# Kernel optimization log

Measured on AMD Instinct MI355X. Metric: run time of the kernel, lower is better.

Reference implementation:

```python
import jax, jax.numpy as jnp
import numpy as np

# ---- dims (match init_kwargs) ----
IMG = 128; PATCH = 16; GRID = IMG // PATCH; L = GRID * GRID  # 64 patches
D = 256            # embed_dim
EXP = 2; DIN = D * EXP          # d_inner = 512
DH = 64; H = DIN // DH          # 8 heads
G = 1; N = 64                   # n_groups, d_state
DCONV = 4
DEPTH = 2
NCLS = 1000
BATCH = 16
DINPROJ = 2 * DIN + 2 * G * N + H   # z | xBC | dt
CDIM = DIN + 2 * G * N              # conv channels
EPS = 1e-6

def _snake_indices():
    g = np.arange(L).reshape(GRID, GRID)
    g[1::2] = g[1::2, ::-1]
    return jnp.asarray(g.reshape(-1))

SNAKE = _snake_indices()

def rmsnorm(x, w):
    return x * jax.lax.rsqrt(jnp.mean(x * x, axis=-1, keepdims=True) + EPS) * w

def causal_depthwise_conv(x, w, b):
    # x: (B,L,C), w: (C,K) depthwise causal conv, then SiLU
    xp = jnp.pad(x, ((0, 0), (DCONV - 1, 0), (0, 0)))
    y = sum(xp[:, k:k + x.shape[1], :] * w[:, k] for k in range(DCONV))
    return jax.nn.silu(y + b)

def mamba_block(x, Win, cw, cb, dtb, Alog, Dp, gn, Wout):
    # Mamba-2/3 style selective scan block. x: (B,L,D)
    Bsz, Lx, _ = x.shape
    zxbcdt = x @ Win                                   # (B,L,DINPROJ)
    z   = zxbcdt[..., :DIN]
    xBC = zxbcdt[..., DIN:DIN + CDIM]
    dt  = jax.nn.softplus(zxbcdt[..., DIN + CDIM:] + dtb)   # (B,L,H)
    xBC = causal_depthwise_conv(xBC, cw, cb)
    xs = xBC[..., :DIN].reshape(Bsz, Lx, H, DH)
    Bm = xBC[..., DIN:DIN + G * N].reshape(Bsz, Lx, G, N)
    Cm = xBC[..., DIN + G * N:].reshape(Bsz, Lx, G, N)
    Bh = jnp.repeat(Bm, H // G, axis=2)                # (B,L,H,N)
    Ch = jnp.repeat(Cm, H // G, axis=2)
    decay = jnp.exp(dt * (-jnp.exp(Alog)))             # (B,L,H) in (0,1)
    dBx = jnp.einsum('blh,blhp,blhn->blhpn', dt, xs, Bh)
    def step(h, inp):
        d, u = inp
        h = d[..., None, None] * h + u
        return h, h
    _, hs = jax.lax.scan(step, jnp.zeros((Bsz, H, DH, N), x.dtype),
                         (jnp.moveaxis(decay, 1, 0), jnp.moveaxis(dBx, 1, 0)))
    hs = jnp.moveaxis(hs, 0, 1)                        # (B,L,H,DH,N)
    y = jnp.einsum('blhpn,blhn->blhp', hs, Ch) + Dp[None, None, :, None] * xs
    y = y.reshape(Bsz, Lx, DIN)
    y = rmsnorm(y * jax.nn.silu(z), gn)                # gated RMSNorm
    return y @ Wout                                    # (B,L,D)

def setup_inputs() -> dict:
    key = jax.random.key(0)
    ks = jax.random.split(key, 24)
    s_in = 1.0 / np.sqrt(D); s_out = 1.0 / np.sqrt(DIN)
    def blk(k):
        kk = jax.random.split(k, 8)
        return dict(
            Win=jax.random.normal(kk[0], (DEPTH, D, DINPROJ)) * s_in,
            cw=jax.random.normal(kk[1], (DEPTH, CDIM, DCONV)) * 0.3,
            cb=jnp.zeros((DEPTH, CDIM)),
            dtb=jax.random.normal(kk[2], (DEPTH, H)) * 0.1,
            Alog=jnp.log(jax.random.uniform(kk[3], (DEPTH, H), minval=1.0, maxval=16.0)),
            Dp=jnp.ones((DEPTH, H)),
            gn=jnp.ones((DEPTH, DIN)),
            Wout=jax.random.normal(kk[4], (DEPTH, DIN, D)) * s_out)
    f = blk(ks[0]); b = blk(ks[1])
    inp = {
        'x': jax.random.normal(ks[2], (BATCH, 3, IMG, IMG), dtype=jnp.float32),
        'patch_w': jax.random.normal(ks[3], (D, 3 * PATCH * PATCH)) * (1.0 / np.sqrt(3 * PATCH * PATCH)),
        'patch_b': jnp.zeros((D,)),
        'pos_embed': jax.random.normal(ks[4], (1, L, D)) * 0.02,
        'norms_w': jnp.ones((DEPTH, D)),
        'final_w': jnp.ones((D,)),
        'head_w': jax.random.normal(ks[5], (D, NCLS)) * (1.0 / np.sqrt(D)),
        'head_b': jnp.zeros((NCLS,)),
    }
    for nm, v in f.items():
        inp[nm + '_f'] = v
    for nm, v in b.items():
        inp[nm + '_b'] = v
    return inp

def reference(x, patch_w, patch_b, pos_embed, norms_w, final_w, head_w, head_b,
              Win_f, cw_f, cb_f, dtb_f, Alog_f, Dp_f, gn_f, Wout_f,
              Win_b, cw_b, cb_b, dtb_b, Alog_b, Dp_b, gn_b, Wout_b):
    Bsz = x.shape[0]
    # patch embed == Conv2d(kernel=stride=PATCH)
    p = x.reshape(Bsz, 3, GRID, PATCH, GRID, PATCH).transpose(0, 2, 4, 1, 3, 5)
    p = p.reshape(Bsz, L, 3 * PATCH * PATCH)
    t = p @ patch_w.T + patch_b                        # (B,L,D)
    t = t + pos_embed[0]
    t = t[:, SNAKE, :]                                 # snake scan order
    for i in range(DEPTH):
        nx = rmsnorm(t, norms_w[i])
        of = mamba_block(nx, Win_f[i], cw_f[i], cb_f[i], dtb_f[i], Alog_f[i], Dp_f[i], gn_f[i], Wout_f[i])
        ob = mamba_block(nx[:, ::-1, :], Win_b[i], cw_b[i], cb_b[i], dtb_b[i], Alog_b[i], Dp_b[i], gn_b[i], Wout_b[i])[:, ::-1, :]
        t = t + 0.5 * (of + ob)                        # drop_path_rate=0 -> identity
    t = rmsnorm(t, final_w)
    t = t.mean(axis=1)
    return t @ head_w + head_b
```

## Files before the change

### kernel.cpp

```cpp
#include <hip/hip_runtime.h>
#include <hip/hip_bf16.h>
#include <math.h>

#define IMG 128
#define PATCH 16
#define L 64
#define D 256
#define DIN 512
#define DH 64
#define H 8
#define NSTATE 64
#define DCONV 4
#define DEPTH 2
#define NCLS 1000
#define BATCH 16
#define DINPROJ 1160
#define CDIM 640
#define EPS 1e-6f

typedef __attribute__((ext_vector_type(8))) short short8;
typedef __attribute__((ext_vector_type(4))) float f32x4;
typedef __attribute__((ext_vector_type(4))) unsigned short us4;
typedef unsigned short ushort_t;

__device__ __forceinline__ int snake_tok(int s){
    int r = s >> 3, c = s & 7;
    return (r & 1) ? (r * 8 + (7 - c)) : (r * 8 + c);
}
__device__ __forceinline__ float silu_f(float x){ return x / (1.f + expf(-x)); }
__device__ __forceinline__ float softplus_f(float x){ return x > 20.f ? x : log1pf(expf(x)); }
__device__ __forceinline__ ushort_t f2b(float f){
    __hip_bfloat16 h = __float2bfloat16(f);
    return *(ushort_t*)&h;
}

__global__ __launch_bounds__(256) void wconv_patch_k(
    const float* __restrict__ Win0, const float* __restrict__ Win1,
    const float* __restrict__ Wout0, const float* __restrict__ Wout1,
    ushort_t* __restrict__ wbuf,
    const float* __restrict__ x, const float* __restrict__ PW,
    float* __restrict__ part)
{
    __shared__ float sm[32][33];
    __shared__ __align__(16) ushort_t As[2][64][40];
    __shared__ __align__(16) ushort_t Bs[2][64][40];
    const int zall = blockIdx.z;
    if (zall < 8){
        int z = zall;
        int R, C; const float* src; ushort_t* dst;
        if (z < 4){
            int layer = z >> 1, dir = z & 1;
            src = (dir ? Win1 : Win0) + (size_t)layer * D * DINPROJ;
            dst = wbuf + (size_t)z * 296960;
            R = D; C = DINPROJ;
        } else {
            int zz = z - 4, layer = zz >> 1, dir = zz & 1;
            src = (dir ? Wout1 : Wout0) + (size_t)layer * DIN * D;
            dst = wbuf + 1187840 + (size_t)zz * 131072;
            R = DIN; C = D;
        }
        int ctiles = (C + 31) >> 5, rtiles = R >> 5;
        if (blockIdx.x >= ctiles || blockIdx.y >= rtiles) return;
        int c0 = blockIdx.x * 32, r0 = blockIdx.y * 32;
        int tx = threadIdx.x & 31, ty = threadIdx.x >> 5;
        #pragma unroll
        for (int k = 0; k < 4; ++k){
            int r = r0 + ty + 8 * k, c = c0 + tx;
            sm[ty + 8 * k][tx] = (c < C) ? src[(size_t)r * C + c] : 0.f;
        }
        __syncthreads();
        #pragma unroll
        for (int k = 0; k < 4; ++k){
            int dr = c0 + ty + 8 * k, dc = r0 + tx;
            if (dr < C) dst[(size_t)dr * R + dc] = f2b(sm[tx][ty + 8 * k]);
        }
        return;
    }
    if (blockIdx.x >= 4) return;
    const int t = threadIdx.x;
    const int n0 = blockIdx.x * 64;
    const int b  = blockIdx.y;
    const int split = zall - 8;
    const int kbase = split * 96;
    const int lrow = t >> 2, lc8 = (t & 3) * 8;
    const int tok = snake_tok(lrow), gy = tok >> 3, gx = tok & 7;
    const float* xb = x + (size_t)b * 3 * IMG * IMG;
    const int wave = t >> 6, lane = t & 63;
    const int wm = (wave >> 1) * 32, wn = (wave & 1) * 32;
    const int fro = lane & 15, fk = (lane >> 4) * 8;

    f32x4 acc[2][2];
    #pragma unroll
    for (int i = 0; i < 2; ++i)
        #pragma unroll
        for (int j = 0; j < 2; ++j) acc[i][j] = (f32x4){0.f,0.f,0.f,0.f};

    short8 areg, breg;
    auto gload = [&](int kk){
        int k = kk + lc8;
        int c = k >> 8, rem = k & 255, py = rem >> 4, px = rem & 15;
        const float* srcA = xb + ((size_t)c * IMG + gy * PATCH + py) * IMG + gx * PATCH + px;
        float4 a0 = *(const float4*)(srcA);
        float4 a1 = *(const float4*)(srcA + 4);
        ushort_t ta[8] = {f2b(a0.x),f2b(a0.y),f2b(a0.z),f2b(a0.w),
                          f2b(a1.x),f2b(a1.y),f2b(a1.z),f2b(a1.w)};
        areg = *(short8*)ta;
        const float* srcB = PW + (size_t)(n0 + lrow) * 768 + kk + lc8;
        float4 b0 = *(const float4*)(srcB);
        float4 b1 = *(const float4*)(srcB + 4);
        ushort_t tb[8] = {f2b(b0.x),f2b(b0.y),f2b(b0.z),f2b(b0.w),
                          f2b(b1.x),f2b(b1.y),f2b(b1.z),f2b(b1.w)};
        breg = *(short8*)tb;
    };
    auto sstore = [&](int buf){
        *(short8*)&As[buf][lrow][lc8] = areg;
        *(short8*)&Bs[buf][lrow][lc8] = breg;
    };

    const int nk = 3;
    gload(kbase); sstore(0);
    __syncthreads();
    for (int kt = 0; kt < nk; ++kt){
        const int buf = kt & 1;
        if (kt + 1 < nk) gload(kbase + (kt + 1) * 32);
        short8 af[2], bfr[2];
        af[0]  = *(const short8*)&As[buf][wm + fro][fk];
        af[1]  = *(const short8*)&As[buf][wm + 16 + fro][fk];
        bfr[0] = *(const short8*)&Bs[buf][wn + fro][fk];
        bfr[1] = *(const short8*)&Bs[buf][wn + 16 + fro][fk];
        #pragma unroll
        for (int i = 0; i < 2; ++i)
            #pragma unroll
            for (int j = 0; j < 2; ++j)
                acc[i][j] = __builtin_amdgcn_mfma_f32_16x16x32_bf16(af[i], bfr[j], acc[i][j], 0, 0, 0);
        if (kt + 1 < nk) sstore(buf ^ 1);
        __syncthreads();
    }
    float* Cp = part + (size_t)split * (BATCH * L * D);
    #pragma unroll
    for (int i = 0; i < 2; ++i){
        #pragma unroll
        for (int j = 0; j < 2; ++j){
            int col = n0 + wn + j * 16 + (lane & 15);
            #pragma unroll
            for (int r = 0; r < 4; ++r){
                int srow = wm + i * 16 + (lane >> 4) * 4 + r;
                Cp[(size_t)(b * 64 + srow) * D + col] = acc[i][j][r];
            }
        }
    }
}

__global__ void patch_red_k(const float* __restrict__ part, const float* __restrict__ pb,
                            const float* __restrict__ pos, float* __restrict__ t){
    int i = blockIdx.x * 256 + threadIdx.x;
    int d = i & (D - 1), s = (i >> 8) & (L - 1);
    float v = 0.f;
    #pragma unroll
    for (int r = 0; r < 8; ++r) v += part[i + r * (BATCH * L * D)];
    t[i] = v + pb[d] + pos[snake_tok(s) * D + d];
}

__global__ __launch_bounds__(256) void gemm_in_k(
    const float* __restrict__ T, const float* __restrict__ nw,
    const ushort_t* __restrict__ B0, const ushort_t* __restrict__ B1,
    const float* __restrict__ cw0, const float* __restrict__ cw1,
    const float* __restrict__ cb0, const float* __restrict__ cb1,
    const float* __restrict__ dtb0, const float* __restrict__ dtb1,
    const float* __restrict__ Al0, const float* __restrict__ Al1,
    float* __restrict__ zb0, float* __restrict__ zb1,
    float* __restrict__ xy0, float* __restrict__ xy1,
    float* __restrict__ bc0, float* __restrict__ bc1,
    float* __restrict__ dts0, float* __restrict__ dts1,
    float* __restrict__ cums0, float* __restrict__ cums1)
{
    __shared__ __align__(16) ushort_t As[64][264];
    __shared__ __align__(16) ushort_t Bs[2][64][40];
    __shared__ float Ctile[64][68];
    const int dir = blockIdx.z;
    const ushort_t* __restrict__ Bw = dir ? B1 : B0;
    const int t = threadIdx.x;
    const int m0 = blockIdx.y * 64, n0 = blockIdx.x * 64;
    const int b = blockIdx.y;
    const int arow = t >> 2;
    const int wave = t >> 6, lane = t & 63;
    const int wm = (wave >> 1) * 32, wn = (wave & 1) * 32;
    const int fro = lane & 15, fk = (lane >> 4) * 8;

    {
        const float* src = T + (size_t)(m0 + arow) * D;
        float ss = 0.f;
        #pragma unroll
        for (int i = 0; i < 16; ++i){
            int c = (t & 3) * 4 + i * 16;
            float4 v = *(const float4*)(src + c);
            ss += v.x*v.x + v.y*v.y + v.z*v.z + v.w*v.w;
        }
        ss += __shfl_xor(ss, 1);
        ss += __shfl_xor(ss, 2);
        float sc = rsqrtf(ss * (1.f / (float)D) + EPS);
        #pragma unroll
        for (int i = 0; i < 16; ++i){
            int c = (t & 3) * 4 + i * 16;
            float4 v = *(const float4*)(src + c);
            float4 w = *(const float4*)(nw + c);
            us4 o = {f2b(v.x*sc*w.x), f2b(v.y*sc*w.y), f2b(v.z*sc*w.z), f2b(v.w*sc*w.w)};
            *(us4*)&As[arow][c] = o;
        }
    }
    const int lrow = t >> 2, lc8 = (t & 3) * 8;
    float4 breg;
    auto gloadB = [&](int kk){
        int gn = n0 + lrow;
        if (gn < DINPROJ) breg = *(const float4*)(Bw + (size_t)gn * D + kk + lc8);
        else breg = make_float4(0.f,0.f,0.f,0.f);
    };
    auto sstoreB = [&](int buf){ *(float4*)&Bs[buf][lrow][lc8] = breg; };

    f32x4 acc[2][2];
    #pragma unroll
    for (int i = 0; i < 2; ++i)
        #pragma unroll
        for (int j = 0; j < 2; ++j) acc[i][j] = (f32x4){0.f,0.f,0.f,0.f};

    gloadB(0); sstoreB(0);
    __syncthreads();
    const int nk = D / 32;
    for (int kt = 0; kt < nk; ++kt){
        const int buf = kt & 1;
        if (kt + 1 < nk) gloadB((kt + 1) * 32);
        short8 af[2], bfr[2];
        af[0]  = *(const short8*)&As[wm + fro][kt * 32 + fk];
        af[1]  = *(const short8*)&As[wm + 16 + fro][kt * 32 + fk];
        bfr[0] = *(const short8*)&Bs[buf][wn + fro][fk];
        bfr[1] = *(const short8*)&Bs[buf][wn + 16 + fro][fk];
        #pragma unroll
        for (int i = 0; i < 2; ++i)
            #pragma unroll
            for (int j = 0; j < 2; ++j)
                acc[i][j] = __builtin_amdgcn_mfma_f32_16x16x32_bf16(af[i], bfr[j], acc[i][j], 0, 0, 0);
        if (kt + 1 < nk) sstoreB(buf ^ 1);
        __syncthreads();
    }

    if (n0 < DIN){
        float* zb = dir ? zb1 : zb0;
        #pragma unroll
        for (int i = 0; i < 2; ++i){
            #pragma unroll
            for (int j = 0; j < 2; ++j){
                int col = n0 + wn + j * 16 + (lane & 15);
                #pragma unroll
                for (int r = 0; r < 4; ++r){
                    int row = m0 + wm + i * 16 + (lane >> 4) * 4 + r;
                    zb[(size_t)row * DIN + col] = acc[i][j][r];
                }
            }
        }
        return;
    }

    #pragma unroll
    for (int i = 0; i < 2; ++i){
        #pragma unroll
        for (int j = 0; j < 2; ++j){
            int lcol = wn + j * 16 + (lane & 15);
            #pragma unroll
            for (int r = 0; r < 4; ++r){
                int lr = wm + i * 16 + (lane >> 4) * 4 + r;
                Ctile[lr][lcol] = acc[i][j][r];
            }
        }
    }
    __syncthreads();

    if (n0 < 1152){
        const float* cw = dir ? cw1 : cw0;
        const float* cb = dir ? cb1 : cb0;
        float* xy = dir ? xy1 : xy0;
        float* bc = dir ? bc1 : bc0;
        const int c = t & 63;
        const int cc = n0 - DIN + c;
        const float w0 = cw[cc * DCONV + 0], w1 = cw[cc * DCONV + 1];
        const float w2 = cw[cc * DCONV + 2], w3 = cw[cc * DCONV + 3];
        const float bb = cb[cc];
        #pragma unroll
        for (int rep = 0; rep < 16; ++rep){
            int s = (t >> 6) + rep * 4;
            float a = bb;
            {
                int sp = s - 3;
                if (sp >= 0) a += w0 * Ctile[dir ? 63 - sp : sp][c];
                sp = s - 2;
                if (sp >= 0) a += w1 * Ctile[dir ? 63 - sp : sp][c];
                sp = s - 1;
                if (sp >= 0) a += w2 * Ctile[dir ? 63 - sp : sp][c];
                a += w3 * Ctile[dir ? 63 - s : s][c];
            }
            float v = silu_f(a);
            if (cc < DIN) xy[(size_t)(b * 64 + s) * DIN + cc] = v;
            else          bc[(size_t)(b * 64 + s) * 128 + (cc - DIN)] = v;
        }
        return;
    }

    {
        const float* dtb = dir ? dtb1 : dtb0;
        const float* Al  = dir ? Al1  : Al0;
        float* dts  = dir ? dts1  : dts0;
        float* cums = dir ? cums1 : cums0;
        int s = t & 63;
        int l = dir ? (63 - s) : s;
        #pragma unroll
        for (int rep = 0; rep < 2; ++rep){
            int h = (t >> 6) + rep * 4;
            float raw = Ctile[l][h] + dtb[h];
            float dt = softplus_f(raw);
            float val = -expf(Al[h]) * dt;
            #pragma unroll
            for (int o = 1; o < 64; o <<= 1){
                float u = __shfl_up(val, o);
                if (s >= o) val += u;
            }
            dts[(size_t)(b * 64 + s) * H + h]  = dt;
            cums[(size_t)(b * 64 + s) * H + h] = val;
        }
    }
}

__global__ __launch_bounds__(512) void yscan2_k(
    const float* __restrict__ bc0, const float* __restrict__ bc1,
    const float* __restrict__ dts0, const float* __restrict__ dts1,
    const float* __restrict__ cums0, const float* __restrict__ cums1,
    const float* __restrict__ Dp0, const float* __restrict__ Dp1,
    const float* __restrict__ zb0, const float* __restrict__ zb1,
    float* __restrict__ xy0, float* __restrict__ xy1,
    float* __restrict__ ssq0, float* __restrict__ ssq1)
{
    __shared__ float Bc[64][65];
    __shared__ float CX[64][65];
    __shared__ float Am[64][65];
    __shared__ float cumS[64], dtS[64];
    __shared__ float ssqp[8][64];
    const int h = blockIdx.x, b = blockIdx.y, dir = blockIdx.z;
    const float* bc   = dir ? bc1   : bc0;
    const float* dts  = dir ? dts1  : dts0;
    const float* cums = dir ? cums1 : cums0;
    const float* Dp   = dir ? Dp1   : Dp0;
    const float* zb   = dir ? zb1   : zb0;
    float* xy  = dir ? xy1  : xy0;
    float* ssq = dir ? ssq1 : ssq0;
    const int t = threadIdx.x;

    if (t < 64){
        cumS[t] = cums[(size_t)(b * L + t) * H + h];
        dtS[t]  = dts[(size_t)(b * L + t) * H + h];
    }
    for (int i = t; i < 4096; i += 512){
        int s = i >> 6, n = i & 63;
        Bc[s][n] = bc[(size_t)(b * L + s) * 128 + n];
        CX[s][n] = bc[(size_t)(b * L + s) * 128 + 64 + n];
    }
    __syncthreads();
    for (int i = t; i < 4096; i += 512){
        int s = i >> 6, j = i & 63;
        float v = 0.f;
        if (j <= s){
            float acc = 0.f;
            #pragma unroll
            for (int n = 0; n < 64; ++n) acc += CX[s][n] * Bc[j][n];
            v = acc * expf(cumS[s] - cumS[j]) * dtS[j];
        }
        Am[s][j] = v;
    }
    __syncthreads();
    for (int i = t; i < 4096; i += 512){
        int j = i >> 6, p = i & 63;
        CX[j][p] = xy[(size_t)(b * L + j) * DIN + h * DH + p];
    }
    __syncthreads();
    {
        const int s = t & 63, pg = t >> 6;
        const int l = dir ? (63 - s) : s;
        const size_t row = (size_t)(b * 64 + l);
        const float dp = Dp[h];
        float acc[8];
        #pragma unroll
        for (int pp = 0; pp < 8; ++pp) acc[pp] = dp * CX[s][pg * 8 + pp];
        #pragma unroll
        for (int j = 0; j < 64; ++j){
            float am = Am[s][j];
            #pragma unroll
            for (int pp = 0; pp < 8; ++pp)
                acc[pp] = fmaf(am, CX[j][pg * 8 + pp], acc[pp]);
        }
        const float* zr = zb + row * DIN + h * DH + pg * 8;
        float4 z0 = *(const float4*)(zr);
        float4 z1 = *(const float4*)(zr + 4);
        float zv[8] = {z0.x, z0.y, z0.z, z0.w, z1.x, z1.y, z1.z, z1.w};
        float g2 = 0.f;
        float gout[8];
        #pragma unroll
        for (int pp = 0; pp < 8; ++pp){
            float g = acc[pp] * silu_f(zv[pp]);
            gout[pp] = g;
            g2 += g * g;
        }
        ssqp[pg][s] = g2;
        float* dst = xy + row * DIN + h * DH + pg * 8;
        *(float4*)(dst)     = make_float4(gout[0], gout[1], gout[2], gout[3]);
        *(float4*)(dst + 4) = make_float4(gout[4], gout[5], gout[6], gout[7]);
    }
    __syncthreads();
    if (t < 64){
        int ll = dir ? (63 - t) : t;
        float v = 0.f;
        #pragma unroll
        for (int q = 0; q < 8; ++q) v += ssqp[q][t];
        ssq[(size_t)(b * 64 + ll) * H + h] = v;
    }
}

__global__ __launch_bounds__(256) void gemm_out_k(
    const float* __restrict__ G0, const float* __restrict__ G1,
    const float* __restrict__ ssq0, const float* __restrict__ ssq1,
    const float* __restrict__ gn0, const float* __restrict__ gn1,
    const ushort_t* __restrict__ B0, const ushort_t* __restrict__ B1,
    float* __restrict__ part)
{
    __shared__ __align__(16) ushort_t As[2][64][40];
    __shared__ __align__(16) ushort_t Bs[2][64][40];
    __shared__ float scl[64];
    const int t = threadIdx.x;
    const int n0 = blockIdx.x * 64, m0 = blockIdx.y * 64;
    const int z = blockIdx.z;
    const int dir = z >> 2;
    const int kbase = (z & 3) * 128;
    const float* __restrict__ G   = dir ? G1   : G0;
    const float* __restrict__ ssq = dir ? ssq1 : ssq0;
    const float* __restrict__ gnw = dir ? gn1  : gn0;
    const ushort_t* __restrict__ B = dir ? B1 : B0;
    const int lrow = t >> 2, lc8 = (t & 3) * 8;
    const int wave = t >> 6, lane = t & 63;
    const int wm = (wave >> 1) * 32, wn = (wave & 1) * 32;
    const int fro = lane & 15, fk = (lane >> 4) * 8;

    if (t < 64){
        const float* sr = ssq + (size_t)(m0 + t) * H;
        float v = (sr[0] + sr[1]) + (sr[2] + sr[3]) + (sr[4] + sr[5]) + (sr[6] + sr[7]);
        scl[t] = rsqrtf(v * (1.f / (float)DIN) + EPS);
    }
    __syncthreads();

    short8 areg; float4 breg;
    auto gload = [&](int kk){
        const float* src = G + (size_t)(m0 + lrow) * DIN + kk + lc8;
        float4 a0 = *(const float4*)(src);
        float4 a1 = *(const float4*)(src + 4);
        const float* gw = gnw + kk + lc8;
        float4 w0 = *(const float4*)(gw);
        float4 w1 = *(const float4*)(gw + 4);
        float sc = scl[lrow];
        ushort_t ta[8] = {f2b(a0.x*sc*w0.x), f2b(a0.y*sc*w0.y), f2b(a0.z*sc*w0.z), f2b(a0.w*sc*w0.w),
                          f2b(a1.x*sc*w1.x), f2b(a1.y*sc*w1.y), f2b(a1.z*sc*w1.z), f2b(a1.w*sc*w1.w)};
        areg = *(short8*)ta;
        breg = *(const float4*)(B + (size_t)(n0 + lrow) * DIN + kk + lc8);
    };
    auto sstore = [&](int buf){
        *(short8*)&As[buf][lrow][lc8] = areg;
        *(float4*)&Bs[buf][lrow][lc8] = breg;
    };

    f32x4 acc[2][2];
    #pragma unroll
    for (int i = 0; i < 2; ++i)
        #pragma unroll
        for (int j = 0; j < 2; ++j) acc[i][j] = (f32x4){0.f,0.f,0.f,0.f};

    const int nk = 4;
    gload(kbase); sstore(0);
    __syncthreads();
    for (int kt = 0; kt < nk; ++kt){
        const int buf = kt & 1;
        if (kt + 1 < nk) gload(kbase + (kt + 1) * 32);
        short8 af[2], bfr[2];
        af[0]  = *(const short8*)&As[buf][wm + fro][fk];
        af[1]  = *(const short8*)&As[buf][wm + 16 + fro][fk];
        bfr[0] = *(const short8*)&Bs[buf][wn + fro][fk];
        bfr[1] = *(const short8*)&Bs[buf][wn + 16 + fro][fk];
        #pragma unroll
        for (int i = 0; i < 2; ++i)
            #pragma unroll
            for (int j = 0; j < 2; ++j)
                acc[i][j] = __builtin_amdgcn_mfma_f32_16x16x32_bf16(af[i], bfr[j], acc[i][j], 0, 0, 0);
        if (kt + 1 < nk) sstore(buf ^ 1);
        __syncthreads();
    }
    float* Cp = part + (size_t)z * (BATCH * L * D);
    #pragma unroll
    for (int i = 0; i < 2; ++i){
        #pragma unroll
        for (int j = 0; j < 2; ++j){
            int col = n0 + wn + j * 16 + (lane & 15);
            #pragma unroll
            for (int r = 0; r < 4; ++r){
                int row = m0 + wm + i * 16 + (lane >> 4) * 4 + r;
                Cp[(size_t)row * D + col] = acc[i][j][r];
            }
        }
    }
}

__global__ void out_red_k(const float* __restrict__ part, float* __restrict__ t){
    int i = blockIdx.x * 256 + threadIdx.x;
    float v = 0.f;
    #pragma unroll
    for (int r = 0; r < 8; ++r) v += part[i + r * (BATCH * L * D)];
    t[i] += 0.5f * v;
}

__global__ void finalmean_k(const float* __restrict__ T, const float* __restrict__ part,
                            const float* __restrict__ fw, float* __restrict__ tm8){
    __shared__ float sm[4];
    int b = blockIdx.x, q = blockIdx.y;
    int d = threadIdx.x;
    float a = 0.f;
    for (int r = 0; r < 8; ++r){
        int row = b * 64 + q * 8 + r;
        size_t o = (size_t)row * D + d;
        float pv = 0.f;
        #pragma unroll
        for (int u = 0; u < 8; ++u) pv += part[o + (size_t)u * (BATCH * L * D)];
        float v = T[o] + 0.5f * pv;
        float ssl = v * v;
        #pragma unroll
        for (int off = 32; off > 0; off >>= 1) ssl += __shfl_down(ssl, off);
        if ((threadIdx.x & 63) == 0) sm[threadIdx.x >> 6] = ssl;
        __syncthreads();
        float ss = sm[0] + sm[1] + sm[2] + sm[3];
        __syncthreads();
        float sc = rsqrtf(ss / (float)D + EPS);
        a += v * sc;
    }
    tm8[(q * BATCH + b) * D + d] = a * (1.f / (float)L) * fw[d];
}

__global__ void head_k(const float* __restrict__ tm8, const float* __restrict__ hw,
                       const float* __restrict__ hb, float* __restrict__ out){
    __shared__ float trs[2][256];
    int i0 = blockIdx.x * 256;
    int mmin = i0 / NCLS;
    int t = threadIdx.x;
    #pragma unroll
    for (int mm = 0; mm < 2; ++mm){
        int m = mmin + mm;
        float v = 0.f;
        if (m < BATCH){
            #pragma unroll
            for (int q = 0; q < 8; ++q)
                v += tm8[(q * BATCH + m) * D + t];
        }
        trs[mm][t] = v;
    }
    __syncthreads();
    int i = i0 + t;
    if (i >= BATCH * NCLS) return;
    int m = i / NCLS, n = i - m * NCLS;
    const float* tr = trs[m - mmin];
    const float* hc = hw + n;
    float a0 = 0.f, a1 = 0.f, a2 = 0.f, a3 = 0.f;
    #pragma unroll 4
    for (int k = 0; k < D; k += 4){
        a0 = fmaf(tr[k],     hc[(size_t)k * NCLS],       a0);
        a1 = fmaf(tr[k + 1], hc[(size_t)(k + 1) * NCLS], a1);
        a2 = fmaf(tr[k + 2], hc[(size_t)(k + 2) * NCLS], a2);
        a3 = fmaf(tr[k + 3], hc[(size_t)(k + 3) * NCLS], a3);
    }
    out[i] = (a0 + a1) + (a2 + a3) + hb[n];
}

extern "C" void kernel_launch(void* const* d_in, const int* in_sizes, int n_in,
                              void* d_out, int out_size, void* d_ws, size_t ws_size,
                              hipStream_t stream){
    (void)in_sizes; (void)n_in; (void)out_size; (void)ws_size;
    const float* x       = (const float*)d_in[0];
    const float* patch_w = (const float*)d_in[1];
    const float* patch_b = (const float*)d_in[2];
    const float* pos     = (const float*)d_in[3];
    const float* norms_w = (const float*)d_in[4];
    const float* final_w = (const float*)d_in[5];
    const float* head_w  = (const float*)d_in[6];
    const float* head_b  = (const float*)d_in[7];
    const float* Win[2]  = {(const float*)d_in[8],  (const float*)d_in[16]};
    const float* cw[2]   = {(const float*)d_in[9],  (const float*)d_in[17]};
    const float* cb[2]   = {(const float*)d_in[10], (const float*)d_in[18]};
    const float* dtb[2]  = {(const float*)d_in[11], (const float*)d_in[19]};
    const float* Alog[2] = {(const float*)d_in[12], (const float*)d_in[20]};
    const float* Dp[2]   = {(const float*)d_in[13], (const float*)d_in[21]};
    const float* gn[2]   = {(const float*)d_in[14], (const float*)d_in[22]};
    const float* Wout[2] = {(const float*)d_in[15], (const float*)d_in[23]};

    float* ws = (float*)d_ws;
    float* t     = ws;
    float* tm8   = t     + 262144;
    float* zb0   = tm8   + 32768;
    float* zb1   = zb0   + 524288;
    float* xy0   = zb1   + 524288;
    float* xy1   = xy0   + 524288;
    float* bc0   = xy1   + 524288;
    float* bc1   = bc0   + 131072;
    float* dts0  = bc1   + 131072;
    float* dts1  = dts0  + 8192;
    float* cum0  = dts1  + 8192;
    float* cum1  = cum0  + 8192;
    float* ssq0  = cum1  + 8192;
    float* ssq1  = ssq0  + 8192;
    float* partP = ssq1  + 8192;
    float* partO = partP + 2097152;
    float* f32end = partO + 2097152;

    ushort_t* wbuf = (ushort_t*)f32end;
    ushort_t* win_bf  = wbuf;
    ushort_t* wout_bf = wbuf + 1187840;

    const int BL = BATCH * L;

    wconv_patch_k<<<dim3(37, 16, 16), 256, 0, stream>>>(
        Win[0], Win[1], Wout[0], Wout[1], wbuf, x, patch_w, partP);
    patch_red_k<<<BL, 256, 0, stream>>>(partP, patch_b, pos, t);

    for (int i = 0; i < DEPTH; ++i){
        const float* cw0  = cw[0]   + (size_t)i * CDIM * DCONV;
        const float* cw1  = cw[1]   + (size_t)i * CDIM * DCONV;
        const float* cb0  = cb[0]   + (size_t)i * CDIM;
        const float* cb1  = cb[1]   + (size_t)i * CDIM;
        const float* dtb0 = dtb[0]  + (size_t)i * H;
        const float* dtb1 = dtb[1]  + (size_t)i * H;
        const float* Al0  = Alog[0] + (size_t)i * H;
        const float* Al1  = Alog[1] + (size_t)i * H;
        const float* Dp0  = Dp[0]   + (size_t)i * H;
        const float* Dp1  = Dp[1]   + (size_t)i * H;
        const float* gn0  = gn[0]   + (size_t)i * DIN;
        const float* gn1  = gn[1]   + (size_t)i * DIN;
        const ushort_t* Wi0 = win_bf  + (size_t)(2 * i + 0) * 296960;
        const ushort_t* Wi1 = win_bf  + (size_t)(2 * i + 1) * 296960;
        const ushort_t* Wo0 = wout_bf + (size_t)(2 * i + 0) * 131072;
        const ushort_t* Wo1 = wout_bf + (size_t)(2 * i + 1) * 131072;

        gemm_in_k<<<dim3(19, 16, 2), 256, 0, stream>>>(
            t, norms_w + i * D, Wi0, Wi1, cw0, cw1, cb0, cb1, dtb0, dtb1,
            Al0, Al1, zb0, zb1, xy0, xy1, bc0, bc1, dts0, dts1, cum0, cum1);
        yscan2_k<<<dim3(H, BATCH, 2), 512, 0, stream>>>(
            bc0, bc1, dts0, dts1, cum0, cum1, Dp0, Dp1, zb0, zb1,
            xy0, xy1, ssq0, ssq1);
        gemm_out_k<<<dim3(4, 16, 8), 256, 0, stream>>>(
            xy0, xy1, ssq0, ssq1, gn0, gn1, Wo0, Wo1, partO);
        if (i == 0)
            out_red_k<<<BL, 256, 0, stream>>>(partO, t);
    }

    finalmean_k<<<dim3(BATCH, 8), 256, 0, stream>>>(t, partO, final_w, tm8);
    head_k<<<(BATCH * NCLS + 255) / 256, 256, 0, stream>>>(
        tm8, head_w, head_b, (float*)d_out);
}
```

Baseline: 130.9 us.

## Fuse all stages into one cooperative persistent kernel with grid syncs

Replaces the sequence of separate kernel launches with a single cooperative persistent kernel. Each phase (weight conversion, patch embed, reduction, in-projection, scan, out-projection, final mean, head) runs as a task loop over blocks, and grid.sync() separates the phases. The goal is to remove launch gaps and per-kernel ramp-up between the many small stages. The scan phase now uses 256 threads with 16 outputs per thread instead of 512 with 8. In exchange, every phase runs at the occupancy allowed by the largest shared-memory user, and grid-wide barriers add their own cost; if the cooperative launch fails, it falls back to separate kernels.

```diff
diff --git a/kernel.cpp b/kernel.cpp
--- a/kernel.cpp
+++ b/kernel.cpp
@@ -1,6 +1,9 @@
 #include <hip/hip_runtime.h>
+#include <hip/hip_cooperative_groups.h>
 #include <hip/hip_bf16.h>
 #include <math.h>
+
+namespace cg = cooperative_groups;
 
 #define IMG 128
 #define PATCH 16
@@ -34,58 +37,57 @@
     return *(ushort_t*)&h;
 }
 
-__global__ __launch_bounds__(256) void wconv_patch_k(
-    const float* __restrict__ Win0, const float* __restrict__ Win1,
-    const float* __restrict__ Wout0, const float* __restrict__ Wout1,
-    ushort_t* __restrict__ wbuf,
-    const float* __restrict__ x, const float* __restrict__ PW,
-    float* __restrict__ part)
-{
-    __shared__ float sm[32][33];
-    __shared__ __align__(16) ushort_t As[2][64][40];
-    __shared__ __align__(16) ushort_t Bs[2][64][40];
-    const int zall = blockIdx.z;
-    if (zall < 8){
-        int z = zall;
-        int R, C; const float* src; ushort_t* dst;
-        if (z < 4){
-            int layer = z >> 1, dir = z & 1;
-            src = (dir ? Win1 : Win0) + (size_t)layer * D * DINPROJ;
-            dst = wbuf + (size_t)z * 296960;
-            R = D; C = DINPROJ;
-        } else {
-            int zz = z - 4, layer = zz >> 1, dir = zz & 1;
-            src = (dir ? Wout1 : Wout0) + (size_t)layer * DIN * D;
-            dst = wbuf + 1187840 + (size_t)zz * 131072;
-            R = DIN; C = D;
-        }
-        int ctiles = (C + 31) >> 5, rtiles = R >> 5;
-        if (blockIdx.x >= ctiles || blockIdx.y >= rtiles) return;
-        int c0 = blockIdx.x * 32, r0 = blockIdx.y * 32;
-        int tx = threadIdx.x & 31, ty = threadIdx.x >> 5;
-        #pragma unroll
-        for (int k = 0; k < 4; ++k){
-            int r = r0 + ty + 8 * k, c = c0 + tx;
-            sm[ty + 8 * k][tx] = (c < C) ? src[(size_t)r * C + c] : 0.f;
-        }
-        __syncthreads();
-        #pragma unroll
-        for (int k = 0; k < 4; ++k){
-            int dr = c0 + ty + 8 * k, dc = r0 + tx;
-            if (dr < C) dst[(size_t)dr * R + dc] = f2b(sm[tx][ty + 8 * k]);
-        }
-        return;
-    }
-    if (blockIdx.x >= 4) return;
-    const int t = threadIdx.x;
-    const int n0 = blockIdx.x * 64;
-    const int b  = blockIdx.y;
-    const int split = zall - 8;
+struct MegaP {
+    const float *x, *patch_w, *patch_b, *pos, *norms_w, *final_w, *head_w, *head_b;
+    const float *Win[2], *cw[2], *cb[2], *dtb[2], *Alog[2], *Dp[2], *gn[2], *Wout[2];
+    float *t, *tm8;
+    float *zb[2], *xy[2], *bcb[2], *dts[2], *cums[2], *ssq[2];
+    float *partP, *partO;
+    ushort_t *win_bf, *wout_bf;
+    float *out;
+};
+
+__device__ void ph_wconv(int task, int tid, unsigned char* SM, const MegaP& p){
+    float (*sm)[33] = (float(*)[33])SM;
+    const float* src; ushort_t* dst; int R, C, ctiles, tile;
+    if (task < 1184){
+        int z = task / 296; tile = task - z * 296;
+        src = p.Win[z & 1] + (size_t)(z >> 1) * D * DINPROJ;
+        dst = p.win_bf + (size_t)z * 296960;
+        R = D; C = DINPROJ; ctiles = 37;
+    } else {
+        int k = task - 1184;
+        int z = k >> 7; tile = k & 127;
+        src = p.Wout[z & 1] + (size_t)(z >> 1) * DIN * D;
+        dst = p.wout_bf + (size_t)z * 131072;
+        R = DIN; C = D; ctiles = 8;
+    }
+    int cx = tile % ctiles, ry = tile / ctiles;
+    int c0 = cx * 32, r0 = ry * 32;
+    int tx = tid & 31, ty = tid >> 5;
+    #pragma unroll
+    for (int k = 0; k < 4; ++k){
+        int r = r0 + ty + 8 * k, c = c0 + tx;
+        sm[ty + 8 * k][tx] = (c < C) ? src[(size_t)r * C + c] : 0.f;
+    }
+    __syncthreads();
+    #pragma unroll
+    for (int k = 0; k < 4; ++k){
+        int dr = c0 + ty + 8 * k, dc = r0 + tx;
+        if (dr < C) dst[(size_t)dr * R + dc] = f2b(sm[tx][ty + 8 * k]);
+    }
+}
+
+__device__ void ph_patch(int task, int tid, unsigned char* SM, const MegaP& p){
+    ushort_t (*As)[64][40] = (ushort_t(*)[64][40])SM;
+    ushort_t (*Bs)[64][40] = (ushort_t(*)[64][40])(SM + 10240);
+    const int xi = task & 3, b = (task >> 2) & 15, split = task >> 6;
+    const int n0 = xi * 64;
     const int kbase = split * 96;
-    const int lrow = t >> 2, lc8 = (t & 3) * 8;
+    const int lrow = tid >> 2, lc8 = (tid & 3) * 8;
     const int tok = snake_tok(lrow), gy = tok >> 3, gx = tok & 7;
-    const float* xb = x + (size_t)b * 3 * IMG * IMG;
-    const int wave = t >> 6, lane = t & 63;
+    const float* xb = p.x + (size_t)b * 3 * IMG * IMG;
+    const int wave = tid >> 6, lane = tid & 63;
     const int wm = (wave >> 1) * 32, wn = (wave & 1) * 32;
     const int fro = lane & 15, fk = (lane >> 4) * 8;
 
@@ -105,7 +107,7 @@
         ushort_t ta[8] = {f2b(a0.x),f2b(a0.y),f2b(a0.z),f2b(a0.w),
                           f2b(a1.x),f2b(a1.y),f2b(a1.z),f2b(a1.w)};
         areg = *(short8*)ta;
-        const float* srcB = PW + (size_t)(n0 + lrow) * 768 + kk + lc8;
+        const float* srcB = p.patch_w + (size_t)(n0 + lrow) * 768 + kk + lc8;
         float4 b0 = *(const float4*)(srcB);
         float4 b1 = *(const float4*)(srcB + 4);
         ushort_t tb[8] = {f2b(b0.x),f2b(b0.y),f2b(b0.z),f2b(b0.w),
@@ -133,10 +135,9 @@
             #pragma unroll
             for (int j = 0; j < 2; ++j)
                 acc[i][j] = __builtin_amdgcn_mfma_f32_16x16x32_bf16(af[i], bfr[j], acc[i][j], 0, 0, 0);
-        if (kt + 1 < nk) sstore(buf ^ 1);
-        __syncthreads();
-    }
-    float* Cp = part + (size_t)split * (BATCH * L * D);
+        if (kt + 1 < nk){ sstore(buf ^ 1); __syncthreads(); }
+    }
+    float* Cp = p.partP + (size_t)split * (BATCH * L * D);
     #pragma unroll
     for (int i = 0; i < 2; ++i){
         #pragma unroll
@@ -151,48 +152,38 @@
     }
 }
 
-__global__ void patch_red_k(const float* __restrict__ part, const float* __restrict__ pb,
-                            const float* __restrict__ pos, float* __restrict__ t){
-    int i = blockIdx.x * 256 + threadIdx.x;
+__device__ void ph_patchred(int task, int tid, const MegaP& p){
+    int i = task * 256 + tid;
     int d = i & (D - 1), s = (i >> 8) & (L - 1);
     float v = 0.f;
     #pragma unroll
-    for (int r = 0; r < 8; ++r) v += part[i + r * (BATCH * L * D)];
-    t[i] = v + pb[d] + pos[snake_tok(s) * D + d];
-}
-
-__global__ __launch_bounds__(256) void gemm_in_k(
-    const float* __restrict__ T, const float* __restrict__ nw,
-    const ushort_t* __restrict__ B0, const ushort_t* __restrict__ B1,
-    const float* __restrict__ cw0, const float* __restrict__ cw1,
-    const float* __restrict__ cb0, const float* __restrict__ cb1,
-    const float* __restrict__ dtb0, const float* __restrict__ dtb1,
-    const float* __restrict__ Al0, const float* __restrict__ Al1,
-    float* __restrict__ zb0, float* __restrict__ zb1,
-    float* __restrict__ xy0, float* __restrict__ xy1,
-    float* __restrict__ bc0, float* __restrict__ bc1,
-    float* __restrict__ dts0, float* __restrict__ dts1,
-    float* __restrict__ cums0, float* __restrict__ cums1)
-{
-    __shared__ __align__(16) ushort_t As[64][264];
-    __shared__ __align__(16) ushort_t Bs[2][64][40];
-    __shared__ float Ctile[64][68];
-    const int dir = blockIdx.z;
-    const ushort_t* __restrict__ Bw = dir ? B1 : B0;
-    const int t = threadIdx.x;
-    const int m0 = blockIdx.y * 64, n0 = blockIdx.x * 64;
-    const int b = blockIdx.y;
-    const int arow = t >> 2;
-    const int wave = t >> 6, lane = t & 63;
+    for (int r = 0; r < 8; ++r) v += p.partP[i + r * (BATCH * L * D)];
+    p.t[i] = v + p.patch_b[d] + p.pos[snake_tok(s) * D + d];
+}
+
+__device__ void ph_gemm_in(int task, int tid, unsigned char* SM, const MegaP& p, int layer){
+    ushort_t (*As)[264]    = (ushort_t(*)[264])SM;
+    ushort_t (*Bs)[64][40] = (ushort_t(*)[64][40])(SM + 33792);
+    float (*Ctile)[68]     = (float(*)[68])(SM + 33792);
+
+    const int xi  = task % 19;
+    const int b   = (task / 19) & 15;
+    const int dir = task / 304;
+    const int n0 = xi * 64, m0 = b * 64;
+    const ushort_t* Bw = p.win_bf + (size_t)(2 * layer + dir) * 296960;
+    const float* nw = p.norms_w + layer * D;
+
+    const int arow = tid >> 2;
+    const int wave = tid >> 6, lane = tid & 63;
     const int wm = (wave >> 1) * 32, wn = (wave & 1) * 32;
     const int fro = lane & 15, fk = (lane >> 4) * 8;
 
     {
-        const float* src = T + (size_t)(m0 + arow) * D;
+        const float* src = p.t + (size_t)(m0 + arow) * D;
         float ss = 0.f;
         #pragma unroll
         for (int i = 0; i < 16; ++i){
-            int c = (t & 3) * 4 + i * 16;
+            int c = (tid & 3) * 4 + i * 16;
             float4 v = *(const float4*)(src + c);
             ss += v.x*v.x + v.y*v.y + v.z*v.z + v.w*v.w;
         }
@@ -201,14 +192,14 @@
         float sc = rsqrtf(ss * (1.f / (float)D) + EPS);
         #pragma unroll
         for (int i = 0; i < 16; ++i){
-            int c = (t & 3) * 4 + i * 16;
+            int c = (tid & 3) * 4 + i * 16;
             float4 v = *(const float4*)(src + c);
             float4 w = *(const float4*)(nw + c);
             us4 o = {f2b(v.x*sc*w.x), f2b(v.y*sc*w.y), f2b(v.z*sc*w.z), f2b(v.w*sc*w.w)};
             *(us4*)&As[arow][c] = o;
         }
     }
-    const int lrow = t >> 2, lc8 = (t & 3) * 8;
+    const int lrow = tid >> 2, lc8 = (tid & 3) * 8;
     float4 breg;
     auto gloadB = [&](int kk){
         int gn = n0 + lrow;
@@ -239,12 +230,12 @@
             #pragma unroll
             for (int j = 0; j < 2; ++j)
                 acc[i][j] = __builtin_amdgcn_mfma_f32_16x16x32_bf16(af[i], bfr[j], acc[i][j], 0, 0, 0);
-        if (kt + 1 < nk) sstoreB(buf ^ 1);
+        if (kt + 1 < nk){ sstoreB(buf ^ 1); }
         __syncthreads();
     }
 
     if (n0 < DIN){
-        float* zb = dir ? zb1 : zb0;
+        float* zb = p.zb[dir];
         #pragma unroll
         for (int i = 0; i < 2; ++i){
             #pragma unroll
@@ -274,19 +265,19 @@
     }
     __syncthreads();
 
-    if (n0 < 1152){
-        const float* cw = dir ? cw1 : cw0;
-        const float* cb = dir ? cb1 : cb0;
-        float* xy = dir ? xy1 : xy0;
-        float* bc = dir ? bc1 : bc0;
-        const int c = t & 63;
+    if (xi < 18){
+        const float* cw = p.cw[dir] + (size_t)layer * CDIM * DCONV;
+        const float* cb = p.cb[dir] + (size_t)layer * CDIM;
+        float* xy = p.xy[dir];
+        float* bc = p.bcb[dir];
+        const int c = tid & 63;
         const int cc = n0 - DIN + c;
         const float w0 = cw[cc * DCONV + 0], w1 = cw[cc * DCONV + 1];
         const float w2 = cw[cc * DCONV + 2], w3 = cw[cc * DCONV + 3];
         const float bb = cb[cc];
         #pragma unroll
         for (int rep = 0; rep < 16; ++rep){
-            int s = (t >> 6) + rep * 4;
+            int s = (tid >> 6) + rep * 4;
             float a = bb;
             {
                 int sp = s - 3;
@@ -305,15 +296,15 @@
     }
 
     {
-        const float* dtb = dir ? dtb1 : dtb0;
-        const float* Al  = dir ? Al1  : Al0;
-        float* dts  = dir ? dts1  : dts0;
-        float* cums = dir ? cums1 : cums0;
-        int s = t & 63;
+        const float* dtb = p.dtb[dir] + layer * H;
+        const float* Al  = p.Alog[dir] + layer * H;
+        float* dts  = p.dts[dir];
+        float* cums = p.cums[dir];
+        int s = tid & 63;
         int l = dir ? (63 - s) : s;
         #pragma unroll
         for (int rep = 0; rep < 2; ++rep){
-            int h = (t >> 6) + rep * 4;
+            int h = (tid >> 6) + rep * 4;
             float raw = Ctile[l][h] + dtb[h];
             float dt = softplus_f(raw);
             float val = -expf(Al[h]) * dt;
@@ -328,41 +319,33 @@
     }
 }
 
-__global__ __launch_bounds__(512) void yscan2_k(
-    const float* __restrict__ bc0, const float* __restrict__ bc1,
-    const float* __restrict__ dts0, const float* __restrict__ dts1,
-    const float* __restrict__ cums0, const float* __restrict__ cums1,
-    const float* __restrict__ Dp0, const float* __restrict__ Dp1,
-    const float* __restrict__ zb0, const float* __restrict__ zb1,
-    float* __restrict__ xy0, float* __restrict__ xy1,
-    float* __restrict__ ssq0, float* __restrict__ ssq1)
-{
-    __shared__ float Bc[64][65];
-    __shared__ float CX[64][65];
-    __shared__ float Am[64][65];
-    __shared__ float cumS[64], dtS[64];
-    __shared__ float ssqp[8][64];
-    const int h = blockIdx.x, b = blockIdx.y, dir = blockIdx.z;
-    const float* bc   = dir ? bc1   : bc0;
-    const float* dts  = dir ? dts1  : dts0;
-    const float* cums = dir ? cums1 : cums0;
-    const float* Dp   = dir ? Dp1   : Dp0;
-    const float* zb   = dir ? zb1   : zb0;
-    float* xy  = dir ? xy1  : xy0;
-    float* ssq = dir ? ssq1 : ssq0;
-    const int t = threadIdx.x;
-
-    if (t < 64){
-        cumS[t] = cums[(size_t)(b * L + t) * H + h];
-        dtS[t]  = dts[(size_t)(b * L + t) * H + h];
-    }
-    for (int i = t; i < 4096; i += 512){
+__device__ void ph_yscan(int task, int tid, unsigned char* SM, const MegaP& p, int layer){
+    float (*Bc)[65] = (float(*)[65])SM;
+    float (*CX)[65] = (float(*)[65])(SM + 16640);
+    float (*Am)[65] = (float(*)[65])(SM + 33280);
+    float* cumS = (float*)(SM + 49920);
+    float* dtS  = (float*)(SM + 50176);
+    float (*ssqp)[64] = (float(*)[64])(SM + 50432);
+    const int h = task & 7, b = (task >> 3) & 15, dir = task >> 7;
+    const float* bc   = p.bcb[dir];
+    const float* dts  = p.dts[dir];
+    const float* cums = p.cums[dir];
+    const float* Dp   = p.Dp[dir] + layer * H;
+    const float* zb   = p.zb[dir];
+    float* xy  = p.xy[dir];
+    float* ssq = p.ssq[dir];
+
+    if (tid < 64){
+        cumS[tid] = cums[(size_t)(b * L + tid) * H + h];
+        dtS[tid]  = dts[(size_t)(b * L + tid) * H + h];
+    }
+    for (int i = tid; i < 4096; i += 256){
         int s = i >> 6, n = i & 63;
         Bc[s][n] = bc[(size_t)(b * L + s) * 128 + n];
         CX[s][n] = bc[(size_t)(b * L + s) * 128 + 64 + n];
     }
     __syncthreads();
-    for (int i = t; i < 4096; i += 512){
+    for (int i = tid; i < 4096; i += 256){
         int s = i >> 6, j = i & 63;
         float v = 0.f;
         if (j <= s){
@@ -374,81 +357,77 @@
         Am[s][j] = v;
     }
     __syncthreads();
-    for (int i = t; i < 4096; i += 512){
-        int j = i >> 6, p = i & 63;
-        CX[j][p] = xy[(size_t)(b * L + j) * DIN + h * DH + p];
+    for (int i = tid; i < 4096; i += 256){
+        int j = i >> 6, pp = i & 63;
+        CX[j][pp] = xy[(size_t)(b * L + j) * DIN + h * DH + pp];
     }
     __syncthreads();
     {
-        const int s = t & 63, pg = t >> 6;
+        const int s = tid & 63, pg = tid >> 6;
         const int l = dir ? (63 - s) : s;
         const size_t row = (size_t)(b * 64 + l);
         const float dp = Dp[h];
-        float acc[8];
-        #pragma unroll
-        for (int pp = 0; pp < 8; ++pp) acc[pp] = dp * CX[s][pg * 8 + pp];
+        float acc[16];
+        #pragma unroll
+        for (int pp = 0; pp < 16; ++pp) acc[pp] = dp * CX[s][pg * 16 + pp];
         #pragma unroll
         for (int j = 0; j < 64; ++j){
             float am = Am[s][j];
             #pragma unroll
-            for (int pp = 0; pp < 8; ++pp)
-                acc[pp] = fmaf(am, CX[j][pg * 8 + pp], acc[pp]);
-        }
-        const float* zr = zb + row * DIN + h * DH + pg * 8;
+            for (int pp = 0; pp < 16; ++pp)
+                acc[pp] = fmaf(am, CX[j][pg * 16 + pp], acc[pp]);
+        }
+        const float* zr = zb + row * DIN + h * DH + pg * 16;
         float4 z0 = *(const float4*)(zr);
         float4 z1 = *(const float4*)(zr + 4);
-        float zv[8] = {z0.x, z0.y, z0.z, z0.w, z1.x, z1.y, z1.z, z1.w};
+        float4 z2 = *(const float4*)(zr + 8);
+        float4 z3 = *(const float4*)(zr + 12);
+        float zv[16] = {z0.x,z0.y,z0.z,z0.w, z1.x,z1.y,z1.z,z1.w,
+                        z2.x,z2.y,z2.z,z2.w, z3.x,z3.y,z3.z,z3.w};
         float g2 = 0.f;
-        float gout[8];
-        #pragma unroll
-        for (int pp = 0; pp < 8; ++pp){
+        float gout[16];
+        #pragma unroll
+        for (int pp = 0; pp < 16; ++pp){
             float g = acc[pp] * silu_f(zv[pp]);
             gout[pp] = g;
             g2 += g * g;
         }
         ssqp[pg][s] = g2;
-        float* dst = xy + row * DIN + h * DH + pg * 8;
-        *(float4*)(dst)     = make_float4(gout[0], gout[1], gout[2], gout[3]);
-        *(float4*)(dst + 4) = make_float4(gout[4], gout[5], gout[6], gout[7]);
-    }
-    __syncthreads();
-    if (t < 64){
-        int ll = dir ? (63 - t) : t;
-        float v = 0.f;
-        #pragma unroll
-        for (int q = 0; q < 8; ++q) v += ssqp[q][t];
+        float* dst = xy + row * DIN + h * DH + pg * 16;
+        *(float4*)(dst)      = make_float4(gout[0],  gout[1],  gout[2],  gout[3]);
+        *(float4*)(dst + 4)  = make_float4(gout[4],  gout[5],  gout[6],  gout[7]);
+        *(float4*)(dst + 8)  = make_float4(gout[8],  gout[9],  gout[10], gout[11]);
+        *(float4*)(dst + 12) = make_float4(gout[12], gout[13], gout[14], gout[15]);
+    }
+    __syncthreads();
+    if (tid < 64){
+        int ll = dir ? (63 - tid) : tid;
+        float v = (ssqp[0][tid] + ssqp[1][tid]) + (ssqp[2][tid] + ssqp[3][tid]);
         ssq[(size_t)(b * 64 + ll) * H + h] = v;
     }
 }
 
-__global__ __launch_bounds__(256) void gemm_out_k(
-    const float* __restrict__ G0, const float* __restrict__ G1,
-    const float* __restrict__ ssq0, const float* __restrict__ ssq1,
-    const float* __restrict__ gn0, const float* __restrict__ gn1,
-    const ushort_t* __restrict__ B0, const ushort_t* __restrict__ B1,
-    float* __restrict__ part)
-{
-    __shared__ __align__(16) ushort_t As[2][64][40];
-    __shared__ __align__(16) ushort_t Bs[2][64][40];
-    __shared__ float scl[64];
-    const int t = threadIdx.x;
-    const int n0 = blockIdx.x * 64, m0 = blockIdx.y * 64;
-    const int z = blockIdx.z;
+__device__ void ph_gemm_out(int task, int tid, unsigned char* SM, const MegaP& p, int layer){
+    ushort_t (*As)[64][40] = (ushort_t(*)[64][40])SM;
+    ushort_t (*Bs)[64][40] = (ushort_t(*)[64][40])(SM + 10240);
+    float* scl = (float*)(SM + 20480);
+    const int xi = task & 3, mb = (task >> 2) & 15, z = task >> 6;
+    const int n0 = xi * 64, m0 = mb * 64;
     const int dir = z >> 2;
     const int kbase = (z & 3) * 128;
-    const float* __restrict__ G   = dir ? G1   : G0;
-    const float* __restrict__ ssq = dir ? ssq1 : ssq0;
-    const float* __restrict__ gnw = dir ? gn1  : gn0;
-    const ushort_t* __restrict__ B = dir ? B1 : B0;
-    const int lrow = t >> 2, lc8 = (t & 3) * 8;
-    const int wave = t >> 6, lane = t & 63;
+    const float* G   = p.xy[dir];
+    const float* ssq = p.ssq[dir];
+    const float* gnw = p.gn[dir] + (size_t)layer * DIN;
+    const ushort_t* B = p.wout_bf + (size_t)(2 * layer + dir) * 131072;
+    const int lrow = tid >> 2, lc8 = (tid & 3) * 8;
+    const int wave = tid >> 6, lane = tid & 63;
     const int wm = (wave >> 1) * 32, wn = (wave & 1) * 32;
     const int fro = lane & 15, fk = (lane >> 4) * 8;
 
-    if (t < 64){
-        const float* sr = ssq + (size_t)(m0 + t) * H;
+    if (tid < 64){
+        const float* sr = ssq + (size_t)(m0 + tid) * H;
         float v = (sr[0] + sr[1]) + (sr[2] + sr[3]) + (sr[4] + sr[5]) + (sr[6] + sr[7]);
-        scl[t] = rsqrtf(v * (1.f / (float)DIN) + EPS);
+        scl[tid] = rsqrtf(v * (1.f / (float)DIN) + EPS);
     }
     __syncthreads();
 
@@ -493,10 +472,9 @@
             #pragma unroll
             for (int j = 0; j < 2; ++j)
                 acc[i][j] = __builtin_amdgcn_mfma_f32_16x16x32_bf16(af[i], bfr[j], acc[i][j], 0, 0, 0);
-        if (kt + 1 < nk) sstore(buf ^ 1);
-        __syncthreads();
-    }
-    float* Cp = part + (size_t)z * (BATCH * L * D);
+        if (kt + 1 < nk){ sstore(buf ^ 1); __syncthreads(); }
+    }
+    float* Cp = p.partO + (size_t)z * (BATCH * L * D);
     #pragma unroll
     for (int i = 0; i < 2; ++i){
         #pragma unroll
@@ -511,46 +489,43 @@
     }
 }
 
-__global__ void out_red_k(const float* __restrict__ part, float* __restrict__ t){
-    int i = blockIdx.x * 256 + threadIdx.x;
+__device__ void ph_outred(int task, int tid, const MegaP& p){
+    int i = task * 256 + tid;
     float v = 0.f;
     #pragma unroll
-    for (int r = 0; r < 8; ++r) v += part[i + r * (BATCH * L * D)];
-    t[i] += 0.5f * v;
-}
-
-__global__ void finalmean_k(const float* __restrict__ T, const float* __restrict__ part,
-                            const float* __restrict__ fw, float* __restrict__ tm8){
-    __shared__ float sm[4];
-    int b = blockIdx.x, q = blockIdx.y;
-    int d = threadIdx.x;
+    for (int r = 0; r < 8; ++r) v += p.partO[i + r * (BATCH * L * D)];
+    p.t[i] += 0.5f * v;
+}
+
+__device__ void ph_finalmean(int task, int tid, unsigned char* SM, const MegaP& p){
+    float* sm4 = (float*)SM;
+    int b = task & 15, q = task >> 4;
+    int d = tid;
     float a = 0.f;
     for (int r = 0; r < 8; ++r){
         int row = b * 64 + q * 8 + r;
         size_t o = (size_t)row * D + d;
         float pv = 0.f;
         #pragma unroll
-        for (int u = 0; u < 8; ++u) pv += part[o + (size_t)u * (BATCH * L * D)];
-        float v = T[o] + 0.5f * pv;
+        for (int u = 0; u < 8; ++u) pv += p.partO[o + (size_t)u * (BATCH * L * D)];
+        float v = p.t[o] + 0.5f * pv;
         float ssl = v * v;
         #pragma unroll
         for (int off = 32; off > 0; off >>= 1) ssl += __shfl_down(ssl, off);
-        if ((threadIdx.x & 63) == 0) sm[threadIdx.x >> 6] = ssl;
+        if ((tid & 63) == 0) sm4[tid >> 6] = ssl;
         __syncthreads();
-        float ss = sm[0] + sm[1] + sm[2] + sm[3];
+        float ss = sm4[0] + sm4[1] + sm4[2] + sm4[3];
         __syncthreads();
         float sc = rsqrtf(ss / (float)D + EPS);
         a += v * sc;
     }
-    tm8[(q * BATCH + b) * D + d] = a * (1.f / (float)L) * fw[d];
-}
-
-__global__ void head_k(const float* __restrict__ tm8, const float* __restrict__ hw,
-                       const float* __restrict__ hb, float* __restrict__ out){
-    __shared__ float trs[2][256];
-    int i0 = blockIdx.x * 256;
+    p.tm8[(q * BATCH + b) * D + d] = a * (1.f / (float)L) * p.final_w[d];
+}
+
+__device__ void ph_head(int task, int tid, unsigned char* SM, const MegaP& p){
+    float (*trs)[256] = (float(*)[256])SM;
+    int i0 = task * 256;
     int mmin = i0 / NCLS;
-    int t = threadIdx.x;
     #pragma unroll
     for (int mm = 0; mm < 2; ++mm){
         int m = mmin + mm;
@@ -558,16 +533,16 @@
         if (m < BATCH){
             #pragma unroll
             for (int q = 0; q < 8; ++q)
-                v += tm8[(q * BATCH + m) * D + t];
-        }
-        trs[mm][t] = v;
-    }
-    __syncthreads();
-    int i = i0 + t;
+                v += p.tm8[(q * BATCH + m) * D + tid];
+        }
+        trs[mm][tid] = v;
+    }
+    __syncthreads();
+    int i = i0 + tid;
     if (i >= BATCH * NCLS) return;
     int m = i / NCLS, n = i - m * NCLS;
     const float* tr = trs[m - mmin];
-    const float* hc = hw + n;
+    const float* hc = p.head_w + n;
     float a0 = 0.f, a1 = 0.f, a2 = 0.f, a3 = 0.f;
     #pragma unroll 4
     for (int k = 0; k < D; k += 4){
@@ -576,90 +551,161 @@
         a2 = fmaf(tr[k + 2], hc[(size_t)(k + 2) * NCLS], a2);
         a3 = fmaf(tr[k + 3], hc[(size_t)(k + 3) * NCLS], a3);
     }
-    out[i] = (a0 + a1) + (a2 + a3) + hb[n];
+    p.out[i] = (a0 + a1) + (a2 + a3) + p.head_b[n];
+}
+
+__global__ __launch_bounds__(256) void mega_k(MegaP p){
+    __shared__ __align__(16) unsigned char SM[51712];
+    cg::grid_group grid = cg::this_grid();
+    const int tid = threadIdx.x;
+    const int nb = gridDim.x;
+
+    for (int task = blockIdx.x; task < 2208; task += nb){
+        if (task < 1696) ph_wconv(task, tid, SM, p);
+        else             ph_patch(task - 1696, tid, SM, p);
+        __syncthreads();
+    }
+    grid.sync();
+    for (int task = blockIdx.x; task < 1024; task += nb)
+        ph_patchred(task, tid, p);
+    grid.sync();
+
+    for (int layer = 0; layer < DEPTH; ++layer){
+        for (int task = blockIdx.x; task < 608; task += nb){
+            ph_gemm_in(task, tid, SM, p, layer);
+            __syncthreads();
+        }
+        grid.sync();
+        for (int task = blockIdx.x; task < 256; task += nb){
+            ph_yscan(task, tid, SM, p, layer);
+            __syncthreads();
+        }
+        grid.sync();
+        for (int task = blockIdx.x; task < 512; task += nb){
+            ph_gemm_out(task, tid, SM, p, layer);
+            __syncthreads();
+        }
+        grid.sync();
+        if (layer == 0){
+            for (int task = blockIdx.x; task < 1024; task += nb)
+                ph_outred(task, tid, p);
+            grid.sync();
+        }
+    }
+
+    for (int task = blockIdx.x; task < 128; task += nb){
+        ph_finalmean(task, tid, SM, p);
+        __syncthreads();
+    }
+    grid.sync();
+    for (int task = blockIdx.x; task < 63; task += nb){
+        ph_head(task, tid, SM, p);
+        __syncthreads();
+    }
+}
+
+__global__ __launch_bounds__(256) void w_phase0(MegaP p){
+    __shared__ __align__(16) unsigned char SM[20480];
+    int task = blockIdx.x;
+    if (task < 1696) ph_wconv(task, threadIdx.x, SM, p);
+    else             ph_patch(task - 1696, threadIdx.x, SM, p);
+}
+__global__ __launch_bounds__(256) void w_patchred(MegaP p){
+    ph_patchred(blockIdx.x, threadIdx.x, p);
+}
+__global__ __launch_bounds__(256) void w_gemm_in(MegaP p, int layer){
+    __shared__ __align__(16) unsigned char SM[51200];
+    ph_gemm_in(blockIdx.x, threadIdx.x, SM, p, layer);
+}
+__global__ __launch_bounds__(256) void w_yscan(MegaP p, int layer){
+    __shared__ __align__(16) unsigned char SM[51712];
+    ph_yscan(blockIdx.x, threadIdx.x, SM, p, layer);
+}
+__global__ __launch_bounds__(256) void w_gemm_out(MegaP p, int layer){
+    __shared__ __align__(16) unsigned char SM[20736];
+    ph_gemm_out(blockIdx.x, threadIdx.x, SM, p, layer);
+}
+__global__ __launch_bounds__(256) void w_outred(MegaP p){
+    ph_outred(blockIdx.x, threadIdx.x, p);
+}
+__global__ __launch_bounds__(256) void w_finalmean(MegaP p){
+    __shared__ __align__(16) unsigned char SM[16];
+    ph_finalmean(blockIdx.x, threadIdx.x, SM, p);
+}
+__global__ __launch_bounds__(256) void w_head(MegaP p){
+    __shared__ __align__(16) unsigned char SM[2048];
+    ph_head(blockIdx.x, threadIdx.x, SM, p);
 }
 
 extern "C" void kernel_launch(void* const* d_in, const int* in_sizes, int n_in,
                               void* d_out, int out_size, void* d_ws, size_t ws_size,
                               hipStream_t stream){
     (void)in_sizes; (void)n_in; (void)out_size; (void)ws_size;
-    const float* x       = (const float*)d_in[0];
-    const float* patch_w = (const float*)d_in[1];
-    const float* patch_b = (const float*)d_in[2];
-    const float* pos     = (const float*)d_in[3];
-    const float* norms_w = (const float*)d_in[4];
-    const float* final_w = (const float*)d_in[5];
-    const float* head_w  = (const float*)d_in[6];
-    const float* head_b  = (const float*)d_in[7];
-    const float* Win[2]  = {(const float*)d_in[8],  (const float*)d_in[16]};
-    const float* cw[2]   = {(const float*)d_in[9],  (const float*)d_in[17]};
-    const float* cb[2]   = {(const float*)d_in[10], (const float*)d_in[18]};
-    const float* dtb[2]  = {(const float*)d_in[11], (const float*)d_in[19]};
-    const float* Alog[2] = {(const float*)d_in[12], (const float*)d_in[20]};
-    const float* Dp[2]   = {(const float*)d_in[13], (const float*)d_in[21]};
-    const float* gn[2]   = {(const float*)d_in[14], (const float*)d_in[22]};
-    const float* Wout[2] = {(const float*)d_in[15], (const float*)d_in[23]};
+    MegaP p;
+    p.x       = (const float*)d_in[0];
+    p.patch_w = (const float*)d_in[1];
+    p.patch_b = (const float*)d_in[2];
+    p.pos     = (const float*)d_in[3];
+    p.norms_w = (const float*)d_in[4];
+    p.final_w = (const float*)d_in[5];
+    p.head_w  = (const float*)d_in[6];
+    p.head_b  = (const float*)d_in[7];
+    p.Win[0]  = (const float*)d_in[8];   p.Win[1]  = (const float*)d_in[16];
+    p.cw[0]   = (const float*)d_in[9];   p.cw[1]   = (const float*)d_in[17];
+    p.cb[0]   = (const float*)d_in[10];  p.cb[1]   = (const float*)d_in[18];
+    p.dtb[0]  = (const float*)d_in[11];  p.dtb[1]  = (const float*)d_in[19];
+    p.Alog[0] = (const float*)d_in[12];  p.Alog[1] = (const float*)d_in[20];
+    p.Dp[0]   = (const float*)d_in[13];  p.Dp[1]   = (const float*)d_in[21];
+    p.gn[0]   = (const float*)d_in[14];  p.gn[1]   = (const float*)d_in[22];
+    p.Wout[0] = (const float*)d_in[15];  p.Wout[1] = (const float*)d_in[23];
 
     float* ws = (float*)d_ws;
-    float* t     = ws;
-    float* tm8   = t     + 262144;
-    float* zb0   = tm8   + 32768;
-    float* zb1   = zb0   + 524288;
-    float* xy0   = zb1   + 524288;
-    float* xy1   = xy0   + 524288;
-    float* bc0   = xy1   + 524288;
-    float* bc1   = bc0   + 131072;
-    float* dts0  = bc1   + 131072;
-    float* dts1  = dts0  + 8192;
-    float* cum0  = dts1  + 8192;
-    float* cum1  = cum0  + 8192;
-    float* ssq0  = cum1  + 8192;
-    float* ssq1  = ssq0  + 8192;
-    float* partP = ssq1  + 8192;
-    float* partO = partP + 2097152;
-    float* f32end = partO + 2097152;
-
-    ushort_t* wbuf = (ushort_t*)f32end;
-    ushort_t* win_bf  = wbuf;
-    ushort_t* wout_bf = wbuf + 1187840;
-
-    const int BL = BATCH * L;
-
-    wconv_patch_k<<<dim3(37, 16, 16), 256, 0, stream>>>(
-        Win[0], Win[1], Wout[0], Wout[1], wbuf, x, patch_w, partP);
-    patch_red_k<<<BL, 256, 0, stream>>>(partP, patch_b, pos, t);
-
-    for (int i = 0; i < DEPTH; ++i){
-        const float* cw0  = cw[0]   + (size_t)i * CDIM * DCONV;
-        const float* cw1  = cw[1]   + (size_t)i * CDIM * DCONV;
-        const float* cb0  = cb[0]   + (size_t)i * CDIM;
-        const float* cb1  = cb[1]   + (size_t)i * CDIM;
-        const float* dtb0 = dtb[0]  + (size_t)i * H;
-        const float* dtb1 = dtb[1]  + (size_t)i * H;
-        const float* Al0  = Alog[0] + (size_t)i * H;
-        const float* Al1  = Alog[1] + (size_t)i * H;
-        const float* Dp0  = Dp[0]   + (size_t)i * H;
-        const float* Dp1  = Dp[1]   + (size_t)i * H;
-        const float* gn0  = gn[0]   + (size_t)i * DIN;
-        const float* gn1  = gn[1]   + (size_t)i * DIN;
-        const ushort_t* Wi0 = win_bf  + (size_t)(2 * i + 0) * 296960;
-        const ushort_t* Wi1 = win_bf  + (size_t)(2 * i + 1) * 296960;
-        const ushort_t* Wo0 = wout_bf + (size_t)(2 * i + 0) * 131072;
-        const ushort_t* Wo1 = wout_bf + (size_t)(2 * i + 1) * 131072;
-
-        gemm_in_k<<<dim3(19, 16, 2), 256, 0, stream>>>(
-            t, norms_w + i * D, Wi0, Wi1, cw0, cw1, cb0, cb1, dtb0, dtb1,
-            Al0, Al1, zb0, zb1, xy0, xy1, bc0, bc1, dts0, dts1, cum0, cum1);
-        yscan2_k<<<dim3(H, BATCH, 2), 512, 0, stream>>>(
-            bc0, bc1, dts0, dts1, cum0, cum1, Dp0, Dp1, zb0, zb1,
-            xy0, xy1, ssq0, ssq1);
-        gemm_out_k<<<dim3(4, 16, 8), 256, 0, stream>>>(
-            xy0, xy1, ssq0, ssq1, gn0, gn1, Wo0, Wo1, partO);
-        if (i == 0)
-            out_red_k<<<BL, 256, 0, stream>>>(partO, t);
-    }
-
-    finalmean_k<<<dim3(BATCH, 8), 256, 0, stream>>>(t, partO, final_w, tm8);
-    head_k<<<(BATCH * NCLS + 255) / 256, 256, 0, stream>>>(
-        tm8, head_w, head_b, (float*)d_out);
-}
+    p.t      = ws;
+    p.tm8    = p.t      + 262144;
+    p.zb[0]  = p.tm8    + 32768;
+    p.zb[1]  = p.zb[0]  + 524288;
+    p.xy[0]  = p.zb[1]  + 524288;
+    p.xy[1]  = p.xy[0]  + 524288;
+    p.bcb[0] = p.xy[1]  + 524288;
+    p.bcb[1] = p.bcb[0] + 131072;
+    p.dts[0] = p.bcb[1] + 131072;
+    p.dts[1] = p.dts[0] + 8192;
+    p.cums[0]= p.dts[1] + 8192;
+    p.cums[1]= p.cums[0]+ 8192;
+    p.ssq[0] = p.cums[1]+ 8192;
+    p.ssq[1] = p.ssq[0] + 8192;
+    p.partP  = p.ssq[1] + 8192;
+    p.partO  = p.partP  + 2097152;
+    float* f32end = p.partO + 2097152;
+    p.win_bf  = (ushort_t*)f32end;
+    p.wout_bf = p.win_bf + 1187840;
+    p.out = (float*)d_out;
+
+    int dev = 0;
+    hipGetDevice(&dev);
+    int coop = 0, ncu = 0, maxb = 0;
+    hipDeviceGetAttribute(&coop, hipDeviceAttributeCooperativeLaunch, dev);
+    hipDeviceGetAttribute(&ncu, hipDeviceAttributeMultiprocessorCount, dev);
+    hipOccupancyMaxActiveBlocksPerMultiprocessor(&maxb, (const void*)mega_k, 256, 0);
+
+    hipError_t st = hipErrorUnknown;
+    if (coop && maxb > 0 && ncu > 0){
+        int nblk = maxb * ncu;
+        if (nblk > 2208) nblk = 2208;
+        void* args[] = { &p };
+        st = hipLaunchCooperativeKernel((void*)mega_k, dim3(nblk), dim3(256), args, 0, stream);
+    }
+    if (st != hipSuccess){
+        w_phase0<<<2208, 256, 0, stream>>>(p);
+        w_patchred<<<1024, 256, 0, stream>>>(p);
+        for (int layer = 0; layer < DEPTH; ++layer){
+            w_gemm_in<<<608, 256, 0, stream>>>(p, layer);
+            w_yscan<<<256, 256, 0, stream>>>(p, layer);
+            w_gemm_out<<<512, 256, 0, stream>>>(p, layer);
+            if (layer == 0)
+                w_outred<<<1024, 256, 0, stream>>>(p);
+        }
+        w_finalmean<<<128, 256, 0, stream>>>(p);
+        w_head<<<63, 256, 0, stream>>>(p);
+    }
+}
```

Result: slower. 492.3 us (+276.0%).
